# Kernel tuning notes

Measured on AMD Instinct MI355X. Metric: run time of the kernel, lower is better.

The kernel has to match this reference:

```python
import jax, jax.numpy as jnp
import numpy as np

B, INDIM, ENC, BOT, DEC = 2048, 20000, 512, 128, 512
EPS = 1e-5


def _bn(x, g, b):
    # BatchNorm1d in training mode: biased batch stats
    m = jnp.mean(x, axis=0)
    v = jnp.mean(jnp.square(x - m), axis=0)
    return (x - m) * jax.lax.rsqrt(v + EPS) * g + b


def setup_inputs() -> dict:
    key = jax.random.key(0)
    ks = jax.random.split(key, 8)
    s = 0.02  # small init scale keeps exp() outputs finite
    return {
        "x": jax.random.uniform(ks[0], (B, INDIM), dtype=jnp.float32),
        "bn0_g": jnp.ones((INDIM,), jnp.float32),
        "bn0_b": jnp.zeros((INDIM,), jnp.float32),
        "enc_W": jax.random.normal(ks[1], (ENC, INDIM), jnp.float32) * s,
        "enc_b": jnp.zeros((ENC,), jnp.float32),
        "bn1_g": jnp.ones((ENC,), jnp.float32),
        "bn1_b": jnp.zeros((ENC,), jnp.float32),
        "bot_W": jax.random.normal(ks[2], (BOT, ENC), jnp.float32) * s,
        "bot_b": jnp.zeros((BOT,), jnp.float32),
        "bn2_g": jnp.ones((BOT,), jnp.float32),
        "bn2_b": jnp.zeros((BOT,), jnp.float32),
        "dec_W": jax.random.normal(ks[3], (DEC, BOT), jnp.float32) * s,
        "dec_b": jnp.zeros((DEC,), jnp.float32),
        "o1_W": jax.random.normal(ks[4], (INDIM, DEC), jnp.float32) * s,
        "o1_b": jnp.zeros((INDIM,), jnp.float32),
        "o2_W": jax.random.normal(ks[5], (INDIM, DEC), jnp.float32) * s,
        "o2_b": jnp.zeros((INDIM,), jnp.float32),
        "o3_W": jax.random.normal(ks[6], (INDIM, DEC), jnp.float32) * s,
        "o3_b": jnp.zeros((INDIM,), jnp.float32),
    }


def reference(x, bn0_g, bn0_b, enc_W, enc_b, bn1_g, bn1_b, bot_W, bot_b,
              bn2_g, bn2_b, dec_W, dec_b, o1_W, o1_b, o2_W, o2_b, o3_W, o3_b):
    # row-sum / median normalization; diag-inverse @ x == x / s[:, None]
    row_sum = jnp.sum(x, axis=1)                     # [B]
    s = row_sum / jnp.median(row_sum)                # [B]
    h = jnp.log1p(x / s[:, None])                    # log(inv(diag(s)) @ x + 1)
    h = _bn(h, bn0_g, bn0_b)
    h = jax.nn.relu(h @ enc_W.T + enc_b)
    h = _bn(h, bn1_g, bn1_b)
    h = jax.nn.relu(h @ bot_W.T + bot_b)
    h = _bn(h, bn2_g, bn2_b)
    h = jax.nn.relu(h @ dec_W.T + dec_b)
    M = jnp.exp(h @ o1_W.T + o1_b)
    M_loss = s[:, None] * M                          # diag(s) @ M
    pai = jax.nn.sigmoid(h @ o2_W.T + o2_b)
    theta = jnp.exp(h @ o3_W.T + o3_b)
    return pai, M, theta, M_loss
```

## Files before the change

### kernel.cpp

```cpp
#include <hip/hip_runtime.h>
#include <hip/hip_bf16.h>
#include <math.h>

#define B_    2048
#define IND   20000
#define ENCN  512
#define BOTN  128
#define DECN  512
#define KP1   20480
#define NP    20224
#define SPLITK 16
#define KSTEP1 20
#define SPLITK2 4
#define BNEPS 1e-5f

typedef __hip_bfloat16 bf16;
typedef __bf16 bf16x8 __attribute__((ext_vector_type(8)));
typedef float f32x4 __attribute__((ext_vector_type(4)));
typedef unsigned short u16;

__device__ __forceinline__ u16 f2bfu(float f) {
  __hip_bfloat16 h = __float2bfloat16(f);
  return *reinterpret_cast<u16*>(&h);
}

__device__ __forceinline__ void st_b64_bf16(void* p, f32x4 v) {
  union { u16 u[4]; uint2 d; } o;
  o.u[0] = f2bfu(v[0]); o.u[1] = f2bfu(v[1]);
  o.u[2] = f2bfu(v[2]); o.u[3] = f2bfu(v[3]);
  *(uint2*)p = o.d;
}

__device__ __forceinline__ void gload_lds16(const bf16* g, bf16* l) {
  __builtin_amdgcn_global_load_lds(
      (const __attribute__((address_space(1))) void*)g,
      (__attribute__((address_space(3))) void*)l, 16, 0, 0);
}

__global__ void rowsum_k(const float* __restrict__ x, float* __restrict__ row_sum) {
  const int row = blockIdx.x;
  const f32x4* xr = (const f32x4*)(x + (size_t)row * IND);
  float s = 0.f;
  for (int i = threadIdx.x; i < IND / 4; i += 256) {
    f32x4 v = xr[i];
    s += (v[0] + v[1]) + (v[2] + v[3]);
  }
#pragma unroll
  for (int o = 32; o > 0; o >>= 1) s += __shfl_down(s, o, 64);
  __shared__ float ws4[4];
  if ((threadIdx.x & 63) == 0) ws4[threadIdx.x >> 6] = s;
  __syncthreads();
  if (threadIdx.x == 0) row_sum[row] = (ws4[0] + ws4[1]) + (ws4[2] + ws4[3]);
}

__global__ void median_scale_k(const float* __restrict__ row_sum,
                               float* __restrict__ sArr, float* __restrict__ invs) {
  __shared__ float v[B_];
  const int tid = threadIdx.x;
  v[tid] = row_sum[tid];
  v[tid + 1024] = row_sum[tid + 1024];
  __syncthreads();
  for (int k = 2; k <= B_; k <<= 1) {
    for (int j = k >> 1; j > 0; j >>= 1) {
      for (int i = tid; i < B_; i += 1024) {
        int ixj = i ^ j;
        if (ixj > i) {
          bool up = ((i & k) == 0);
          float a = v[i], b = v[ixj];
          if ((a > b) == up) { v[i] = b; v[ixj] = a; }
        }
      }
      __syncthreads();
    }
  }
  float med = 0.5f * (v[B_ / 2 - 1] + v[B_ / 2]);
  for (int i = tid; i < B_; i += 1024) {
    float rs = row_sum[i];
    sArr[i] = rs / med;
    invs[i] = med / rs;
  }
}

__global__ void pass2_k(const float* __restrict__ x, const float* __restrict__ invs,
                        bf16* __restrict__ L, float* __restrict__ part_s,
                        float* __restrict__ part_q) {
  const int c0 = (blockIdx.x * 256 + threadIdx.x) * 4;
  const int rblk = blockIdx.y;
  const int r0 = rblk * 32;
  const bool valid = (c0 < IND);
  f32x4 sum = {0.f, 0.f, 0.f, 0.f}, sq = {0.f, 0.f, 0.f, 0.f};
  for (int r = r0; r < r0 + 32; ++r) {
    f32x4 lv = {0.f, 0.f, 0.f, 0.f};
    if (valid) {
      f32x4 v = *(const f32x4*)(x + (size_t)r * IND + c0);
      float iv = invs[r];
      lv[0] = log1pf(v[0] * iv); lv[1] = log1pf(v[1] * iv);
      lv[2] = log1pf(v[2] * iv); lv[3] = log1pf(v[3] * iv);
      sum += lv; sq += lv * lv;
    }
    ushort4 o;
    o.x = f2bfu(lv[0]); o.y = f2bfu(lv[1]); o.z = f2bfu(lv[2]); o.w = f2bfu(lv[3]);
    *(ushort4*)((u16*)L + (size_t)r * KP1 + c0) = o;
  }
  if (valid) {
    *(f32x4*)(part_s + (size_t)rblk * KP1 + c0) = sum;
    *(f32x4*)(part_q + (size_t)rblk * KP1 + c0) = sq;
  }
}

__global__ void finalize_bn_k(const float* __restrict__ part_s, const float* __restrict__ part_q,
                              const float* __restrict__ g, const float* __restrict__ b,
                              float* __restrict__ scale, float* __restrict__ shift) {
  int c = blockIdx.x * 256 + threadIdx.x;
  if (c >= IND) return;
  float s = 0.f, q = 0.f;
  for (int z = 0; z < 64; ++z) {
    s += part_s[(size_t)z * KP1 + c];
    q += part_q[(size_t)z * KP1 + c];
  }
  const float invN = 1.f / (float)B_;
  float mean = s * invN;
  float var = q * invN - mean * mean;
  float sc = g[c] * rsqrtf(var + BNEPS);
  scale[c] = sc;
  shift[c] = b[c] - mean * sc;
}

__global__ void prepw_k(const float* __restrict__ encW, const float* __restrict__ enc_b,
                        const float* __restrict__ scale0, const float* __restrict__ shift0,
                        bf16* __restrict__ Wp, float* __restrict__ bias1) {
  const int e = blockIdx.x;
  float local = 0.f;
  for (int j0 = threadIdx.x * 4; j0 < KP1; j0 += 1024) {
    ushort4 o;
    if (j0 < IND) {
      f32x4 w = *(const f32x4*)(encW + (size_t)e * IND + j0);
      f32x4 sc = *(const f32x4*)(scale0 + j0);
      f32x4 sh = *(const f32x4*)(shift0 + j0);
      local += sh[0] * w[0] + sh[1] * w[1] + sh[2] * w[2] + sh[3] * w[3];
      o.x = f2bfu(w[0] * sc[0]); o.y = f2bfu(w[1] * sc[1]);
      o.z = f2bfu(w[2] * sc[2]); o.w = f2bfu(w[3] * sc[3]);
    } else {
      o.x = 0; o.y = 0; o.z = 0; o.w = 0;
    }
    *(ushort4*)((u16*)Wp + (size_t)e * KP1 + j0) = o;
  }
#pragma unroll
  for (int o = 32; o > 0; o >>= 1) local += __shfl_down(local, o, 64);
  __shared__ float red[4];
  if ((threadIdx.x & 63) == 0) red[threadIdx.x >> 6] = local;
  __syncthreads();
  if (threadIdx.x == 0) bias1[e] = enc_b[e] + ((red[0] + red[1]) + (red[2] + red[3]));
}

__global__ __launch_bounds__(512, 2)
void gemm1_k(const bf16* __restrict__ A, const bf16* __restrict__ Bm,
             float* __restrict__ Cp) {
  extern __shared__ __align__(16) bf16 smem[];
  bf16* Asm = smem;
  bf16* Bsm = smem + 32768;
  const int tid = threadIdx.x;
  const int lane = tid & 63;
  const int wave = tid >> 6;
  const int wr = wave >> 2;
  const int wc = wave & 3;

  const int bid = blockIdx.x;
  const int swz = (bid & 7) * 32 + (bid >> 3);
  const int xm = swz & 7;
  const int rest = swz >> 3;
  const int yn = rest & 1;
  const int z = rest >> 1;
  const int m0 = xm * 256;
  const int n0 = yn * 256;
  const int kbeg = z * KSTEP1 * 64;

  const int srow = tid >> 3;
  const int schunk = (tid & 7) ^ (srow & 7);
  const bf16* gA = A + (size_t)(m0 + srow) * KP1 + kbeg + schunk * 8;
  const bf16* gB = Bm + (size_t)(n0 + srow) * KP1 + kbeg + schunk * 8;
  const int dst1 = tid * 8;

  const int lrow = lane & 15;
  const int kq = lane >> 4;
  const int rsw = lrow & 7;

  f32x4 acc[8][4] = {};
  bf16x8 bfv[4][2];

  auto SA = [&](int kt, int half) {
    const bf16* g = gA + (size_t)(half * 128) * KP1 + (size_t)kt * 64;
    bf16* l = Asm + (((kt & 1) * 2 + half) << 13) + dst1;
    gload_lds16(g, l);
    gload_lds16(g + (size_t)64 * KP1, l + 4096);
  };
  auto SB = [&](int kt, int half) {
    const bf16* g = gB + (size_t)(half * 128) * KP1 + (size_t)kt * 64;
    bf16* l = Bsm + (((kt & 1) * 2 + half) << 13) + dst1;
    gload_lds16(g, l);
    gload_lds16(g + (size_t)64 * KP1, l + 4096);
  };
  auto DSA = [&](int slot, int p, bf16x8 af[2][2]) {
#pragma unroll
    for (int i = 0; i < 2; ++i) {
      const int m = 2 * p + i;
      const int base = ((slot * 2 + (m >> 2)) * 128 + (m & 3) * 32 + wr * 16 + lrow) * 64;
#pragma unroll
      for (int kk = 0; kk < 2; ++kk)
        af[i][kk] = *(const bf16x8*)(&Asm[base + (((kk * 4 + kq) ^ rsw) << 3)]);
    }
  };
  auto DSB = [&](int slot) {
#pragma unroll
    for (int n = 0; n < 4; ++n) {
      const int base = ((slot * 2 + (wc >> 1)) * 128 + (wc & 1) * 64 + n * 16 + lrow) * 64;
#pragma unroll
      for (int kk = 0; kk < 2; ++kk)
        bfv[n][kk] = *(const bf16x8*)(&Bsm[base + (((kk * 4 + kq) ^ rsw) << 3)]);
    }
  };
  auto MF = [&](int p, bf16x8 af[2][2]) {
    __builtin_amdgcn_s_setprio(1);
#pragma unroll
    for (int i = 0; i < 2; ++i)
#pragma unroll
      for (int n = 0; n < 4; ++n)
#pragma unroll
        for (int kk = 0; kk < 2; ++kk)
          acc[2 * p + i][n] = __builtin_amdgcn_mfma_f32_16x16x32_bf16(
              bfv[n][kk], af[i][kk], acc[2 * p + i][n], 0, 0, 0);
    __builtin_amdgcn_s_setprio(0);
  };

  SA(0, 0); SA(0, 1); SB(0, 0); SB(0, 1);
  SB(1, 0); SB(1, 1); SA(1, 0);
  asm volatile("s_waitcnt vmcnt(6)" ::: "memory");
  __builtin_amdgcn_s_barrier();

  const int iters = KSTEP1 >> 1;
  for (int t = 0; t < iters; ++t) {
    const int e = 2 * t;
    const bool last = (t == iters - 1);
    bf16x8 af[2][2];
    DSB(0); DSA(0, 0, af);
    SA(e + 1, 1);
    __builtin_amdgcn_s_barrier();
    MF(0, af);
    __builtin_amdgcn_s_barrier();
    DSA(0, 1, af);
    if (!last) SB(e + 2, 0);
    __builtin_amdgcn_s_barrier();
    MF(1, af);
    __builtin_amdgcn_s_barrier();
    DSA(0, 2, af);
    if (!last) SB(e + 2, 1);
    __builtin_amdgcn_s_barrier();
    MF(2, af);
    __builtin_amdgcn_s_barrier();
    DSA(0, 3, af);
    if (!last) SA(e + 2, 0);
    if (last) { asm volatile("s_waitcnt vmcnt(0)" ::: "memory"); }
    else      { asm volatile("s_waitcnt vmcnt(6)" ::: "memory"); }
    __builtin_amdgcn_s_barrier();
    MF(3, af);
    __builtin_amdgcn_s_barrier();
    DSB(1); DSA(1, 0, af);
    if (!last) SA(e + 2, 1);
    __builtin_amdgcn_s_barrier();
    MF(0, af);
    __builtin_amdgcn_s_barrier();
    DSA(1, 1, af);
    if (!last) SB(e + 3, 0);
    __builtin_amdgcn_s_barrier();
    MF(1, af);
    __builtin_amdgcn_s_barrier();
    DSA(1, 2, af);
    if (!last) SB(e + 3, 1);
    __builtin_amdgcn_s_barrier();
    MF(2, af);
    __builtin_amdgcn_s_barrier();
    DSA(1, 3, af);
    if (!last) SA(e + 3, 0);
    if (last) { asm volatile("s_waitcnt vmcnt(0)" ::: "memory"); }
    else      { asm volatile("s_waitcnt vmcnt(6)" ::: "memory"); }
    __builtin_amdgcn_s_barrier();
    MF(3, af);
    __builtin_amdgcn_s_barrier();
  }

  float* o0 = Cp + (size_t)z * ((size_t)B_ * ENCN);
  const int gcolb = n0 + wc * 64 + kq * 4;
#pragma unroll
  for (int m = 0; m < 8; ++m) {
    const int grow = m0 + m * 32 + wr * 16 + lrow;
#pragma unroll
    for (int n = 0; n < 4; ++n) {
      const int gcol = gcolb + n * 16;
      *(f32x4*)(&o0[(size_t)grow * ENCN + gcol]) = acc[m][n];
    }
  }
}

__global__ __launch_bounds__(512, 2)
void gemm_out_k(const bf16* __restrict__ A, const bf16* __restrict__ Wall,
                const float* __restrict__ b0, const float* __restrict__ b1,
                const float* __restrict__ b2,
                const float* __restrict__ sArr, float* __restrict__ out) {
  extern __shared__ __align__(16) bf16 smem[];
  bf16* Asm = smem;
  bf16* Bsm = smem + 32768;
  const int tid = threadIdx.x;
  const int lane = tid & 63;
  const int wave = tid >> 6;
  const int wr = wave >> 2;
  const int wc = wave & 3;

  const int bid = blockIdx.x;
  const int swz = (bid & 7) * 237 + (bid >> 3);
  const int g = swz / 632;
  const int r2 = swz - g * 632;
  const int xm = r2 & 7;
  const int yn = r2 >> 3;
  const int m0 = xm * 256;
  const int n0 = yn * 256;

  const bf16* Bm = Wall + (size_t)g * ((size_t)NP * ENCN);
  const float* bg = (g == 0) ? b0 : (g == 1) ? b1 : b2;
  const size_t OFF = (size_t)B_ * IND;
  float* o0 = out + (size_t)g * OFF;
  float* o1 = out + 3 * OFF;

  const int srow = tid >> 3;
  const int schunk = (tid & 7) ^ (srow & 7);
  const bf16* gA = A + (size_t)(m0 + srow) * ENCN + schunk * 8;
  const bf16* gB = Bm + (size_t)(n0 + srow) * ENCN + schunk * 8;
  const int dst1 = tid * 8;

  const int lrow = lane & 15;
  const int kq = lane >> 4;
  const int rsw = lrow & 7;

  f32x4 acc[8][4] = {};
  bf16x8 bfv[4][2];

  auto SA = [&](int kt, int half) {
    const bf16* g_ = gA + (size_t)(half * 128) * ENCN + (size_t)kt * 64;
    bf16* l = Asm + (((kt & 1) * 2 + half) << 13) + dst1;
    gload_lds16(g_, l);
    gload_lds16(g_ + (size_t)64 * ENCN, l + 4096);
  };
  auto SB = [&](int kt, int half) {
    const bf16* g_ = gB + (size_t)(half * 128) * ENCN + (size_t)kt * 64;
    bf16* l = Bsm + (((kt & 1) * 2 + half) << 13) + dst1;
    gload_lds16(g_, l);
    gload_lds16(g_ + (size_t)64 * ENCN, l + 4096);
  };
  auto DSA = [&](int slot, int p, bf16x8 af[2][2]) {
#pragma unroll
    for (int i = 0; i < 2; ++i) {
      const int m = 2 * p + i;
      const int base = ((slot * 2 + (m >> 2)) * 128 + (m & 3) * 32 + wr * 16 + lrow) * 64;
#pragma unroll
      for (int kk = 0; kk < 2; ++kk)
        af[i][kk] = *(const bf16x8*)(&Asm[base + (((kk * 4 + kq) ^ rsw) << 3)]);
    }
  };
  auto DSB = [&](int slot) {
#pragma unroll
    for (int n = 0; n < 4; ++n) {
      const int base = ((slot * 2 + (wc >> 1)) * 128 + (wc & 1) * 64 + n * 16 + lrow) * 64;
#pragma unroll
      for (int kk = 0; kk < 2; ++kk)
        bfv[n][kk] = *(const bf16x8*)(&Bsm[base + (((kk * 4 + kq) ^ rsw) << 3)]);
    }
  };
  auto MF = [&](int p, bf16x8 af[2][2]) {
    __builtin_amdgcn_s_setprio(1);
#pragma unroll
    for (int i = 0; i < 2; ++i)
#pragma unroll
      for (int n = 0; n < 4; ++n)
#pragma unroll
        for (int kk = 0; kk < 2; ++kk)
          acc[2 * p + i][n] = __builtin_amdgcn_mfma_f32_16x16x32_bf16(
              bfv[n][kk], af[i][kk], acc[2 * p + i][n], 0, 0, 0);
    __builtin_amdgcn_s_setprio(0);
  };

  SA(0, 0); SA(0, 1); SB(0, 0); SB(0, 1);
  SB(1, 0); SB(1, 1); SA(1, 0);
  asm volatile("s_waitcnt vmcnt(6)" ::: "memory");
  __builtin_amdgcn_s_barrier();

  const int iters = 4;
  for (int t = 0; t < iters; ++t) {
    const int e = 2 * t;
    const bool last = (t == iters - 1);
    bf16x8 af[2][2];
    DSB(0); DSA(0, 0, af);
    SA(e + 1, 1);
    __builtin_amdgcn_s_barrier();
    MF(0, af);
    __builtin_amdgcn_s_barrier();
    DSA(0, 1, af);
    if (!last) SB(e + 2, 0);
    __builtin_amdgcn_s_barrier();
    MF(1, af);
    __builtin_amdgcn_s_barrier();
    DSA(0, 2, af);
    if (!last) SB(e + 2, 1);
    __builtin_amdgcn_s_barrier();
    MF(2, af);
    __builtin_amdgcn_s_barrier();
    DSA(0, 3, af);
    if (!last) SA(e + 2, 0);
    if (last) { asm volatile("s_waitcnt vmcnt(0)" ::: "memory"); }
    else      { asm volatile("s_waitcnt vmcnt(6)" ::: "memory"); }
    __builtin_amdgcn_s_barrier();
    MF(3, af);
    __builtin_amdgcn_s_barrier();
    DSB(1); DSA(1, 0, af);
    if (!last) SA(e + 2, 1);
    __builtin_amdgcn_s_barrier();
    MF(0, af);
    __builtin_amdgcn_s_barrier();
    DSA(1, 1, af);
    if (!last) SB(e + 3, 0);
    __builtin_amdgcn_s_barrier();
    MF(1, af);
    __builtin_amdgcn_s_barrier();
    DSA(1, 2, af);
    if (!last) SB(e + 3, 1);
    __builtin_amdgcn_s_barrier();
    MF(2, af);
    __builtin_amdgcn_s_barrier();
    DSA(1, 3, af);
    if (!last) SA(e + 3, 0);
    if (last) { asm volatile("s_waitcnt vmcnt(0)" ::: "memory"); }
    else      { asm volatile("s_waitcnt vmcnt(6)" ::: "memory"); }
    __builtin_amdgcn_s_barrier();
    MF(3, af);
    __builtin_amdgcn_s_barrier();
  }

  const int gcolb = n0 + wc * 64 + kq * 4;
#pragma unroll
  for (int m = 0; m < 8; ++m) {
    const int grow = m0 + m * 32 + wr * 16 + lrow;
    float srow_s = 0.f;
    if (g == 1) srow_s = sArr[grow];
#pragma unroll
    for (int n = 0; n < 4; ++n) {
      const int gcol = gcolb + n * 16;
      if (gcol < IND) {
        f32x4 bb = *(const f32x4*)(&bg[gcol]);
        f32x4 t = acc[m][n] + bb;
        f32x4 r;
        if (g == 0) {
#pragma unroll
          for (int j = 0; j < 4; ++j) r[j] = 1.f / (1.f + __expf(-t[j]));
          *(f32x4*)(&o0[(size_t)grow * IND + gcol]) = r;
        } else {
#pragma unroll
          for (int j = 0; j < 4; ++j) r[j] = __expf(t[j]);
          *(f32x4*)(&o0[(size_t)grow * IND + gcol]) = r;
          if (g == 1) {
            f32x4 rl;
#pragma unroll
            for (int j = 0; j < 4; ++j) rl[j] = srow_s * r[j];
            *(f32x4*)(&o1[(size_t)grow * IND + gcol]) = rl;
          }
        }
      }
    }
  }
}

template <int EPI>
__global__ __launch_bounds__(256, 2)
void gemm_mid_k(const float* __restrict__ A, int lda,
                const float* __restrict__ scl, const float* __restrict__ sft,
                const float* __restrict__ W, int ldb,
                const float* __restrict__ bias,
                float* __restrict__ outP, bf16* __restrict__ outB, int ldo) {
  __shared__ __align__(16) bf16 As[128 * 64];
  __shared__ __align__(16) bf16 Bs[128 * 64];
  const int tid = threadIdx.x;
  const int lane = tid & 63;
  const int wave = tid >> 6;
  const int wr = wave >> 1, wc = wave & 1;
  const int m0 = blockIdx.x * 128;
  const int n0 = blockIdx.y * 128;
  const int z = blockIdx.z;
  const int kbeg = z * 128;
  const int lrow = lane & 15;
  const int kq = lane >> 4;
  const int scol = lrow * 4;
  const int srow0 = wave * 32 + kq;

  f32x4 acc[4][4] = {};
  for (int ks = 0; ks < 2; ++ks) {
    const int kb = kbeg + ks * 64;
    f32x4 sc4 = *(const f32x4*)(scl + kb + scol);
    f32x4 sf4 = *(const f32x4*)(sft + kb + scol);
#pragma unroll
    for (int i = 0; i < 8; ++i) {
      const int r = srow0 + i * 4;
      const int byte = r * 128 + (((lrow >> 1) ^ (r & 7)) << 4) + ((lrow & 1) << 3);
      f32x4 a = *(const f32x4*)(A + (size_t)(m0 + r) * lda + kb + scol);
      a = a * sc4 + sf4;
      st_b64_bf16((char*)As + byte, a);
      f32x4 b = *(const f32x4*)(W + (size_t)(n0 + r) * ldb + kb + scol);
      st_b64_bf16((char*)Bs + byte, b);
    }
    __syncthreads();
#pragma unroll
    for (int kk = 0; kk < 2; ++kk) {
      const int kc = kk * 4 + kq;
      bf16x8 af[4], bfv[4];
#pragma unroll
      for (int m = 0; m < 4; ++m) {
        const int row = wr * 64 + m * 16 + lrow;
        af[m] = *(const bf16x8*)(&As[row * 64 + (((kc ^ (row & 7)) & 7) << 3)]);
      }
#pragma unroll
      for (int n = 0; n < 4; ++n) {
        const int row = wc * 64 + n * 16 + lrow;
        bfv[n] = *(const bf16x8*)(&Bs[row * 64 + (((kc ^ (row & 7)) & 7) << 3)]);
      }
#pragma unroll
      for (int m = 0; m < 4; ++m)
#pragma unroll
        for (int n = 0; n < 4; ++n)
          acc[m][n] = __builtin_amdgcn_mfma_f32_16x16x32_bf16(bfv[n], af[m], acc[m][n], 0, 0, 0);
    }
    __syncthreads();
  }

  const int growb = m0 + wr * 64 + lrow;
  const int gcolb = n0 + wc * 64 + kq * 4;
#pragma unroll
  for (int m = 0; m < 4; ++m) {
    const int grow = growb + m * 16;
#pragma unroll
    for (int n = 0; n < 4; ++n) {
      const int gcol = gcolb + n * 16;
      if (EPI == 0) {
        float* op = outP + (size_t)z * ((size_t)B_ * ldo);
        *(f32x4*)(&op[(size_t)grow * ldo + gcol]) = acc[m][n];
      } else {
        f32x4 t = acc[m][n] + *(const f32x4*)(&bias[gcol]);
        f32x4 r;
#pragma unroll
        for (int j = 0; j < 4; ++j) r[j] = fmaxf(t[j], 0.f);
        st_b64_bf16((u16*)outB + (size_t)grow * ldo + gcol, r);
      }
    }
  }
}

__global__ void reduce1c_k(const float* __restrict__ Cp, const float* __restrict__ bias1,
                           float* __restrict__ C1, float* __restrict__ ps,
                           float* __restrict__ pq) {
  const int b = blockIdx.x;
  const int t = threadIdx.x;
  const int c4 = (t & 127) * 4;
  const int rs = t >> 7;
  f32x4 bb = *(const f32x4*)(bias1 + c4);
  f32x4 sum = {0.f, 0.f, 0.f, 0.f}, sq = {0.f, 0.f, 0.f, 0.f};
#pragma unroll
  for (int rr = 0; rr < 4; ++rr) {
    const int row = b * 8 + rs + rr * 2;
    f32x4 v = {0.f, 0.f, 0.f, 0.f};
#pragma unroll
    for (int z = 0; z < SPLITK; ++z)
      v += *(const f32x4*)(Cp + (size_t)z * (B_ * ENCN) + (size_t)row * ENCN + c4);
    v += bb;
    f32x4 r;
#pragma unroll
    for (int j = 0; j < 4; ++j) r[j] = fmaxf(v[j], 0.f);
    *(f32x4*)(C1 + (size_t)row * ENCN + c4) = r;
    sum += r; sq += r * r;
  }
  __shared__ f32x4 ls[2][128], lq[2][128];
  ls[rs][t & 127] = sum; lq[rs][t & 127] = sq;
  __syncthreads();
  if (t < 128) {
    f32x4 s = ls[0][t] + ls[1][t];
    f32x4 q = lq[0][t] + lq[1][t];
    *(f32x4*)(ps + (size_t)b * ENCN + t * 4) = s;
    *(f32x4*)(pq + (size_t)b * ENCN + t * 4) = q;
  }
}

__global__ void reduce2c_k(const float* __restrict__ Cp2, const float* __restrict__ bias,
                           float* __restrict__ C2, float* __restrict__ ps,
                           float* __restrict__ pq) {
  const int b = blockIdx.x;
  const int t = threadIdx.x;
  const int c4 = (t & 31) * 4;
  const int rs = t >> 5;
  f32x4 bb = *(const f32x4*)(bias + c4);
  f32x4 sum = {0.f, 0.f, 0.f, 0.f}, sq = {0.f, 0.f, 0.f, 0.f};
#pragma unroll
  for (int rr = 0; rr < 2; ++rr) {
    const int row = b * 16 + rs + rr * 8;
    f32x4 v = {0.f, 0.f, 0.f, 0.f};
#pragma unroll
    for (int z = 0; z < SPLITK2; ++z)
      v += *(const f32x4*)(Cp2 + (size_t)z * (B_ * BOTN) + (size_t)row * BOTN + c4);
    v += bb;
    f32x4 r;
#pragma unroll
    for (int j = 0; j < 4; ++j) r[j] = fmaxf(v[j], 0.f);
    *(f32x4*)(C2 + (size_t)row * BOTN + c4) = r;
    sum += r; sq += r * r;
  }
  __shared__ f32x4 ls[8][32], lq[8][32];
  ls[rs][t & 31] = sum; lq[rs][t & 31] = sq;
  __syncthreads();
  if (t < 32) {
    f32x4 s = {0.f, 0.f, 0.f, 0.f}, q = {0.f, 0.f, 0.f, 0.f};
#pragma unroll
    for (int k = 0; k < 8; ++k) { s += ls[k][t]; q += lq[k][t]; }
    *(f32x4*)(ps + (size_t)b * BOTN + t * 4) = s;
    *(f32x4*)(pq + (size_t)b * BOTN + t * 4) = q;
  }
}

__global__ void colfin_k(const float* __restrict__ ps, const float* __restrict__ pq,
                         const float* __restrict__ g, const float* __restrict__ b,
                         float* __restrict__ scale, float* __restrict__ shift,
                         int C, int nPart) {
  const int cl = threadIdx.x & 63;
  const int pg = threadIdx.x >> 6;
  const int c = blockIdx.x * 64 + cl;
  float s = 0.f, q = 0.f;
  for (int p = pg; p < nPart; p += 4) {
    s += ps[(size_t)p * C + c];
    q += pq[(size_t)p * C + c];
  }
  __shared__ float ls[4][64], lq[4][64];
  ls[pg][cl] = s; lq[pg][cl] = q;
  __syncthreads();
  if (pg == 0) {
    s = (ls[0][cl] + ls[1][cl]) + (ls[2][cl] + ls[3][cl]);
    q = (lq[0][cl] + lq[1][cl]) + (lq[2][cl] + lq[3][cl]);
    const float invN = 1.f / (float)B_;
    float mean = s * invN;
    float var = q * invN - mean * mean;
    float sc = g[c] * rsqrtf(var + BNEPS);
    scale[c] = sc;
    shift[c] = b[c] - mean * sc;
  }
}

__global__ void cvt_all_k(const float* __restrict__ W0, const float* __restrict__ W1,
                          const float* __restrict__ W2, bf16* __restrict__ Wb) {
  const size_t SEG = (size_t)NP * 512;
  const size_t idx = ((size_t)blockIdx.x * 256 + threadIdx.x) * 4;
  const int seg = (int)(idx / SEG);
  const size_t rem = idx - (size_t)seg * SEG;
  const int e = (int)(rem >> 9);
  const float* src = (seg == 0) ? W0 : (seg == 1) ? W1 : W2;
  ushort4 o;
  if (e < IND) {
    f32x4 v = *(const f32x4*)(src + rem);
    o.x = f2bfu(v[0]); o.y = f2bfu(v[1]); o.z = f2bfu(v[2]); o.w = f2bfu(v[3]);
  } else {
    o.x = 0; o.y = 0; o.z = 0; o.w = 0;
  }
  *(ushort4*)((u16*)Wb + idx) = o;
}

extern "C" void kernel_launch(void* const* d_in, const int* in_sizes, int n_in,
                              void* d_out, int out_size, void* d_ws, size_t ws_size,
                              hipStream_t stream) {
  const float* x     = (const float*)d_in[0];
  const float* bn0_g = (const float*)d_in[1];
  const float* bn0_b = (const float*)d_in[2];
  const float* enc_W = (const float*)d_in[3];
  const float* enc_b = (const float*)d_in[4];
  const float* bn1_g = (const float*)d_in[5];
  const float* bn1_b = (const float*)d_in[6];
  const float* bot_W = (const float*)d_in[7];
  const float* bot_b = (const float*)d_in[8];
  const float* bn2_g = (const float*)d_in[9];
  const float* bn2_b = (const float*)d_in[10];
  const float* dec_W = (const float*)d_in[11];
  const float* dec_b = (const float*)d_in[12];
  const float* o1_W  = (const float*)d_in[13];
  const float* o1_b  = (const float*)d_in[14];
  const float* o2_W  = (const float*)d_in[15];
  const float* o2_b  = (const float*)d_in[16];
  const float* o3_W  = (const float*)d_in[17];
  const float* o3_b  = (const float*)d_in[18];

  char* wsb = (char*)d_ws;
  size_t off = 0;
  auto alloc = [&](size_t bytes) -> void* {
    void* p = wsb + off;
    off = (off + bytes + 255) & ~(size_t)255;
    return p;
  };
  float* row_sum = (float*)alloc(B_ * 4);
  float* sArr    = (float*)alloc(B_ * 4);
  float* invs    = (float*)alloc(B_ * 4);
  float* scale0  = (float*)alloc(IND * 4);
  float* shift0  = (float*)alloc(IND * 4);
  float* bias1   = (float*)alloc(ENCN * 4);
  float* scale1  = (float*)alloc(ENCN * 4);
  float* shift1  = (float*)alloc(ENCN * 4);
  float* scale2  = (float*)alloc(BOTN * 4);
  float* shift2  = (float*)alloc(BOTN * 4);
  float* ps1     = (float*)alloc(256 * ENCN * 4);
  float* pq1     = (float*)alloc(256 * ENCN * 4);
  float* ps2     = (float*)alloc(128 * BOTN * 4);
  float* pq2     = (float*)alloc(128 * BOTN * 4);
  float* C1      = (float*)alloc((size_t)B_ * ENCN * 4);
  float* C2f     = (float*)alloc((size_t)B_ * BOTN * 4);
  float* Cp2     = (float*)alloc((size_t)SPLITK2 * B_ * BOTN * 4);
  float* Cp      = (float*)alloc((size_t)SPLITK * B_ * ENCN * 4);
  bf16*  L       = (bf16*)alloc((size_t)B_ * KP1 * 2);
  bf16*  Wp      = (bf16*)alloc((size_t)ENCN * KP1 * 2);
  bf16*  h3      = (bf16*)alloc((size_t)B_ * DECN * 2);
  bf16*  Wall    = (bf16*)alloc((size_t)3 * NP * 512 * 2);
  float* part_s  = Cp;
  float* part_q  = Cp + (size_t)64 * KP1;

  hipFuncSetAttribute(reinterpret_cast<const void*>(gemm1_k),
                      hipFuncAttributeMaxDynamicSharedMemorySize, 131072);
  hipFuncSetAttribute(reinterpret_cast<const void*>(gemm_out_k),
                      hipFuncAttributeMaxDynamicSharedMemorySize, 131072);

  rowsum_k<<<B_, 256, 0, stream>>>(x, row_sum);
  median_scale_k<<<1, 1024, 0, stream>>>(row_sum, sArr, invs);

  pass2_k<<<dim3(KP1 / 1024, 64), 256, 0, stream>>>(x, invs, L, part_s, part_q);
  finalize_bn_k<<<(IND + 255) / 256, 256, 0, stream>>>(part_s, part_q, bn0_g, bn0_b,
                                                       scale0, shift0);

  prepw_k<<<ENCN, 256, 0, stream>>>(enc_W, enc_b, scale0, shift0, Wp, bias1);

  gemm1_k<<<256, 512, 131072, stream>>>(L, Wp, Cp);
  reduce1c_k<<<256, 256, 0, stream>>>(Cp, bias1, C1, ps1, pq1);
  colfin_k<<<ENCN / 64, 256, 0, stream>>>(ps1, pq1, bn1_g, bn1_b, scale1, shift1,
                                          ENCN, 256);

  gemm_mid_k<0><<<dim3(16, 1, SPLITK2), 256, 0, stream>>>(
      C1, ENCN, scale1, shift1, bot_W, ENCN, nullptr, Cp2, nullptr, BOTN);
  reduce2c_k<<<128, 256, 0, stream>>>(Cp2, bot_b, C2f, ps2, pq2);
  colfin_k<<<BOTN / 64, 256, 0, stream>>>(ps2, pq2, bn2_g, bn2_b, scale2, shift2,
                                          BOTN, 128);
  gemm_mid_k<1><<<dim3(16, 4, 1), 256, 0, stream>>>(
      C2f, BOTN, scale2, shift2, dec_W, BOTN, dec_b, nullptr, h3, DECN);

  cvt_all_k<<<(3 * NP * 512) / 1024, 256, 0, stream>>>(o2_W, o1_W, o3_W, Wall);

  float* out = (float*)d_out;
  gemm_out_k<<<1896, 512, 131072, stream>>>(h3, Wall, o2_b, o1_b, o3_b, sArr, out);
}
```

Measured before the change: 681.0 us.

## Fuse output weight conversion into pass2, split output GEMM per head, rank-based median

Folds the bf16 conversion of the three output weight matrices into the log1p/BN-stats kernel as extra blocks, so both memory-bound passes share one launch. The first GEMM and the output GEMM now use one templated kernel, and the single combined output GEMM becomes three launches, one per head. The bitonic sort in the median kernel is replaced by an O(N) rank count per element with a single barrier. Separate per-head launches add tail and launch overhead, and the combined pass2 kernel has more uneven per-block work.

```diff
diff --git a/kernel.cpp b/kernel.cpp
--- a/kernel.cpp
+++ b/kernel.cpp
@@ -13,6 +13,7 @@
 #define KSTEP1 20
 #define SPLITK2 4
 #define BNEPS 1e-5f
+#define WSEG  (NP * 512)
 
 typedef __hip_bfloat16 bf16;
 typedef __bf16 bf16x8 __attribute__((ext_vector_type(8)));
@@ -56,55 +57,81 @@
 __global__ void median_scale_k(const float* __restrict__ row_sum,
                                float* __restrict__ sArr, float* __restrict__ invs) {
   __shared__ float v[B_];
+  __shared__ float mv[2];
   const int tid = threadIdx.x;
   v[tid] = row_sum[tid];
   v[tid + 1024] = row_sum[tid + 1024];
   __syncthreads();
-  for (int k = 2; k <= B_; k <<= 1) {
-    for (int j = k >> 1; j > 0; j >>= 1) {
-      for (int i = tid; i < B_; i += 1024) {
-        int ixj = i ^ j;
-        if (ixj > i) {
-          bool up = ((i & k) == 0);
-          float a = v[i], b = v[ixj];
-          if ((a > b) == up) { v[i] = b; v[ixj] = a; }
-        }
-      }
-      __syncthreads();
-    }
-  }
-  float med = 0.5f * (v[B_ / 2 - 1] + v[B_ / 2]);
+  const float a = v[tid];
+  const float b = v[tid + 1024];
+  int ra = 0, rb = 0;
+  for (int j = 0; j < B_; ++j) {
+    float x = v[j];
+    ra += (x < a) | ((x == a) & (j < tid));
+    rb += (x < b) | ((x == b) & (j < tid + 1024));
+  }
+  if (ra == 1023) mv[0] = a;
+  if (ra == 1024) mv[1] = a;
+  if (rb == 1023) mv[0] = b;
+  if (rb == 1024) mv[1] = b;
+  __syncthreads();
+  const float med = 0.5f * (mv[0] + mv[1]);
   for (int i = tid; i < B_; i += 1024) {
-    float rs = row_sum[i];
+    float rs = v[i];
     sArr[i] = rs / med;
     invs[i] = med / rs;
   }
 }
 
-__global__ void pass2_k(const float* __restrict__ x, const float* __restrict__ invs,
-                        bf16* __restrict__ L, float* __restrict__ part_s,
-                        float* __restrict__ part_q) {
-  const int c0 = (blockIdx.x * 256 + threadIdx.x) * 4;
-  const int rblk = blockIdx.y;
-  const int r0 = rblk * 32;
-  const bool valid = (c0 < IND);
-  f32x4 sum = {0.f, 0.f, 0.f, 0.f}, sq = {0.f, 0.f, 0.f, 0.f};
-  for (int r = r0; r < r0 + 32; ++r) {
-    f32x4 lv = {0.f, 0.f, 0.f, 0.f};
+__global__ void pass2cvt_k(const float* __restrict__ x, const float* __restrict__ invs,
+                           bf16* __restrict__ L, float* __restrict__ part_s,
+                           float* __restrict__ part_q,
+                           const float* __restrict__ W0, const float* __restrict__ W1,
+                           const float* __restrict__ W2, bf16* __restrict__ Wall) {
+  const int b = blockIdx.x;
+  if (b < 1280) {
+    const int bx = b % 20;
+    const int rblk = b / 20;
+    const int c0 = (bx * 256 + threadIdx.x) * 4;
+    const int r0 = rblk * 32;
+    const bool valid = (c0 < IND);
+    f32x4 sum = {0.f, 0.f, 0.f, 0.f}, sq = {0.f, 0.f, 0.f, 0.f};
+    for (int r = r0; r < r0 + 32; ++r) {
+      f32x4 lv = {0.f, 0.f, 0.f, 0.f};
+      if (valid) {
+        f32x4 v = *(const f32x4*)(x + (size_t)r * IND + c0);
+        float iv = invs[r];
+        lv[0] = log1pf(v[0] * iv); lv[1] = log1pf(v[1] * iv);
+        lv[2] = log1pf(v[2] * iv); lv[3] = log1pf(v[3] * iv);
+        sum += lv; sq += lv * lv;
+      }
+      ushort4 o;
+      o.x = f2bfu(lv[0]); o.y = f2bfu(lv[1]); o.z = f2bfu(lv[2]); o.w = f2bfu(lv[3]);
+      *(ushort4*)((u16*)L + (size_t)r * KP1 + c0) = o;
+    }
     if (valid) {
-      f32x4 v = *(const f32x4*)(x + (size_t)r * IND + c0);
-      float iv = invs[r];
-      lv[0] = log1pf(v[0] * iv); lv[1] = log1pf(v[1] * iv);
-      lv[2] = log1pf(v[2] * iv); lv[3] = log1pf(v[3] * iv);
-      sum += lv; sq += lv * lv;
-    }
-    ushort4 o;
-    o.x = f2bfu(lv[0]); o.y = f2bfu(lv[1]); o.z = f2bfu(lv[2]); o.w = f2bfu(lv[3]);
-    *(ushort4*)((u16*)L + (size_t)r * KP1 + c0) = o;
-  }
-  if (valid) {
-    *(f32x4*)(part_s + (size_t)rblk * KP1 + c0) = sum;
-    *(f32x4*)(part_q + (size_t)rblk * KP1 + c0) = sq;
+      *(f32x4*)(part_s + (size_t)rblk * KP1 + c0) = sum;
+      *(f32x4*)(part_q + (size_t)rblk * KP1 + c0) = sq;
+    }
+  } else {
+    const long long TC = (long long)3 * WSEG / 4;
+    long long idx = (long long)(b - 1280) * 256 + threadIdx.x;
+    const long long stride = 1024 * 256;
+    for (; idx < TC; idx += stride) {
+      const long long e4 = idx * 4;
+      const int seg = (int)(e4 / WSEG);
+      const long long rem = e4 - (long long)seg * WSEG;
+      const int erow = (int)(rem >> 9);
+      const float* src = (seg == 0) ? W0 : (seg == 1) ? W1 : W2;
+      ushort4 o;
+      if (erow < IND) {
+        f32x4 v = *(const f32x4*)(src + rem);
+        o.x = f2bfu(v[0]); o.y = f2bfu(v[1]); o.z = f2bfu(v[2]); o.w = f2bfu(v[3]);
+      } else {
+        o.x = 0; o.y = 0; o.z = 0; o.w = 0;
+      }
+      *(ushort4*)((u16*)Wall + e4) = o;
+    }
   }
 }
 
@@ -153,9 +180,13 @@
   if (threadIdx.x == 0) bias1[e] = enc_b[e] + ((red[0] + red[1]) + (red[2] + red[3]));
 }
 
+template <int MODE>
 __global__ __launch_bounds__(512, 2)
-void gemm1_k(const bf16* __restrict__ A, const bf16* __restrict__ Bm,
-             float* __restrict__ Cp) {
+void gemm256(const bf16* __restrict__ A, const bf16* __restrict__ Bm,
+             int Kpad, int ksteps,
+             float* __restrict__ out0, float* __restrict__ out1,
+             const float* __restrict__ bias, const float* __restrict__ sArr,
+             int ldo, int Nlimit) {
   extern __shared__ __align__(16) bf16 smem[];
   bf16* Asm = smem;
   bf16* Bsm = smem + 32768;
@@ -165,20 +196,22 @@
   const int wr = wave >> 2;
   const int wc = wave & 3;
 
+  const int nwg = gridDim.x;
+  const int q8 = nwg >> 3;
   const int bid = blockIdx.x;
-  const int swz = (bid & 7) * 32 + (bid >> 3);
+  const int swz = (bid & 7) * q8 + (bid >> 3);
   const int xm = swz & 7;
   const int rest = swz >> 3;
-  const int yn = rest & 1;
-  const int z = rest >> 1;
+  int yn, z;
+  if (MODE == 0) { yn = rest & 1; z = rest >> 1; } else { yn = rest; z = 0; }
   const int m0 = xm * 256;
   const int n0 = yn * 256;
-  const int kbeg = z * KSTEP1 * 64;
+  const int kbeg = z * ksteps * 64;
 
   const int srow = tid >> 3;
   const int schunk = (tid & 7) ^ (srow & 7);
-  const bf16* gA = A + (size_t)(m0 + srow) * KP1 + kbeg + schunk * 8;
-  const bf16* gB = Bm + (size_t)(n0 + srow) * KP1 + kbeg + schunk * 8;
+  const bf16* gA = A + (size_t)(m0 + srow) * Kpad + kbeg + schunk * 8;
+  const bf16* gB = Bm + (size_t)(n0 + srow) * Kpad + kbeg + schunk * 8;
   const int dst1 = tid * 8;
 
   const int lrow = lane & 15;
@@ -189,16 +222,16 @@
   bf16x8 bfv[4][2];
 
   auto SA = [&](int kt, int half) {
-    const bf16* g = gA + (size_t)(half * 128) * KP1 + (size_t)kt * 64;
+    const bf16* g = gA + (size_t)(half * 128) * Kpad + (size_t)kt * 64;
     bf16* l = Asm + (((kt & 1) * 2 + half) << 13) + dst1;
     gload_lds16(g, l);
-    gload_lds16(g + (size_t)64 * KP1, l + 4096);
+    gload_lds16(g + (size_t)64 * Kpad, l + 4096);
   };
   auto SB = [&](int kt, int half) {
-    const bf16* g = gB + (size_t)(half * 128) * KP1 + (size_t)kt * 64;
+    const bf16* g = gB + (size_t)(half * 128) * Kpad + (size_t)kt * 64;
     bf16* l = Bsm + (((kt & 1) * 2 + half) << 13) + dst1;
     gload_lds16(g, l);
-    gload_lds16(g + (size_t)64 * KP1, l + 4096);
+    gload_lds16(g + (size_t)64 * Kpad, l + 4096);
   };
   auto DSA = [&](int slot, int p, bf16x8 af[2][2]) {
 #pragma unroll
@@ -237,7 +270,7 @@
   asm volatile("s_waitcnt vmcnt(6)" ::: "memory");
   __builtin_amdgcn_s_barrier();
 
-  const int iters = KSTEP1 >> 1;
+  const int iters = ksteps >> 1;
   for (int t = 0; t < iters; ++t) {
     const int e = 2 * t;
     const bool last = (t == iters - 1);
@@ -288,188 +321,40 @@
     __builtin_amdgcn_s_barrier();
   }
 
-  float* o0 = Cp + (size_t)z * ((size_t)B_ * ENCN);
-  const int gcolb = n0 + wc * 64 + kq * 4;
-#pragma unroll
-  for (int m = 0; m < 8; ++m) {
-    const int grow = m0 + m * 32 + wr * 16 + lrow;
-#pragma unroll
-    for (int n = 0; n < 4; ++n) {
-      const int gcol = gcolb + n * 16;
-      *(f32x4*)(&o0[(size_t)grow * ENCN + gcol]) = acc[m][n];
-    }
-  }
-}
-
-__global__ __launch_bounds__(512, 2)
-void gemm_out_k(const bf16* __restrict__ A, const bf16* __restrict__ Wall,
-                const float* __restrict__ b0, const float* __restrict__ b1,
-                const float* __restrict__ b2,
-                const float* __restrict__ sArr, float* __restrict__ out) {
-  extern __shared__ __align__(16) bf16 smem[];
-  bf16* Asm = smem;
-  bf16* Bsm = smem + 32768;
-  const int tid = threadIdx.x;
-  const int lane = tid & 63;
-  const int wave = tid >> 6;
-  const int wr = wave >> 2;
-  const int wc = wave & 3;
-
-  const int bid = blockIdx.x;
-  const int swz = (bid & 7) * 237 + (bid >> 3);
-  const int g = swz / 632;
-  const int r2 = swz - g * 632;
-  const int xm = r2 & 7;
-  const int yn = r2 >> 3;
-  const int m0 = xm * 256;
-  const int n0 = yn * 256;
-
-  const bf16* Bm = Wall + (size_t)g * ((size_t)NP * ENCN);
-  const float* bg = (g == 0) ? b0 : (g == 1) ? b1 : b2;
-  const size_t OFF = (size_t)B_ * IND;
-  float* o0 = out + (size_t)g * OFF;
-  float* o1 = out + 3 * OFF;
-
-  const int srow = tid >> 3;
-  const int schunk = (tid & 7) ^ (srow & 7);
-  const bf16* gA = A + (size_t)(m0 + srow) * ENCN + schunk * 8;
-  const bf16* gB = Bm + (size_t)(n0 + srow) * ENCN + schunk * 8;
-  const int dst1 = tid * 8;
-
-  const int lrow = lane & 15;
-  const int kq = lane >> 4;
-  const int rsw = lrow & 7;
-
-  f32x4 acc[8][4] = {};
-  bf16x8 bfv[4][2];
-
-  auto SA = [&](int kt, int half) {
-    const bf16* g_ = gA + (size_t)(half * 128) * ENCN + (size_t)kt * 64;
-    bf16* l = Asm + (((kt & 1) * 2 + half) << 13) + dst1;
-    gload_lds16(g_, l);
-    gload_lds16(g_ + (size_t)64 * ENCN, l + 4096);
-  };
-  auto SB = [&](int kt, int half) {
-    const bf16* g_ = gB + (size_t)(half * 128) * ENCN + (size_t)kt * 64;
-    bf16* l = Bsm + (((kt & 1) * 2 + half) << 13) + dst1;
-    gload_lds16(g_, l);
-    gload_lds16(g_ + (size_t)64 * ENCN, l + 4096);
-  };
-  auto DSA = [&](int slot, int p, bf16x8 af[2][2]) {
-#pragma unroll
-    for (int i = 0; i < 2; ++i) {
-      const int m = 2 * p + i;
-      const int base = ((slot * 2 + (m >> 2)) * 128 + (m & 3) * 32 + wr * 16 + lrow) * 64;
-#pragma unroll
-      for (int kk = 0; kk < 2; ++kk)
-        af[i][kk] = *(const bf16x8*)(&Asm[base + (((kk * 4 + kq) ^ rsw) << 3)]);
-    }
-  };
-  auto DSB = [&](int slot) {
-#pragma unroll
-    for (int n = 0; n < 4; ++n) {
-      const int base = ((slot * 2 + (wc >> 1)) * 128 + (wc & 1) * 64 + n * 16 + lrow) * 64;
-#pragma unroll
-      for (int kk = 0; kk < 2; ++kk)
-        bfv[n][kk] = *(const bf16x8*)(&Bsm[base + (((kk * 4 + kq) ^ rsw) << 3)]);
-    }
-  };
-  auto MF = [&](int p, bf16x8 af[2][2]) {
-    __builtin_amdgcn_s_setprio(1);
-#pragma unroll
-    for (int i = 0; i < 2; ++i)
-#pragma unroll
-      for (int n = 0; n < 4; ++n)
-#pragma unroll
-        for (int kk = 0; kk < 2; ++kk)
-          acc[2 * p + i][n] = __builtin_amdgcn_mfma_f32_16x16x32_bf16(
-              bfv[n][kk], af[i][kk], acc[2 * p + i][n], 0, 0, 0);
-    __builtin_amdgcn_s_setprio(0);
-  };
-
-  SA(0, 0); SA(0, 1); SB(0, 0); SB(0, 1);
-  SB(1, 0); SB(1, 1); SA(1, 0);
-  asm volatile("s_waitcnt vmcnt(6)" ::: "memory");
-  __builtin_amdgcn_s_barrier();
-
-  const int iters = 4;
-  for (int t = 0; t < iters; ++t) {
-    const int e = 2 * t;
-    const bool last = (t == iters - 1);
-    bf16x8 af[2][2];
-    DSB(0); DSA(0, 0, af);
-    SA(e + 1, 1);
-    __builtin_amdgcn_s_barrier();
-    MF(0, af);
-    __builtin_amdgcn_s_barrier();
-    DSA(0, 1, af);
-    if (!last) SB(e + 2, 0);
-    __builtin_amdgcn_s_barrier();
-    MF(1, af);
-    __builtin_amdgcn_s_barrier();
-    DSA(0, 2, af);
-    if (!last) SB(e + 2, 1);
-    __builtin_amdgcn_s_barrier();
-    MF(2, af);
-    __builtin_amdgcn_s_barrier();
-    DSA(0, 3, af);
-    if (!last) SA(e + 2, 0);
-    if (last) { asm volatile("s_waitcnt vmcnt(0)" ::: "memory"); }
-    else      { asm volatile("s_waitcnt vmcnt(6)" ::: "memory"); }
-    __builtin_amdgcn_s_barrier();
-    MF(3, af);
-    __builtin_amdgcn_s_barrier();
-    DSB(1); DSA(1, 0, af);
-    if (!last) SA(e + 2, 1);
-    __builtin_amdgcn_s_barrier();
-    MF(0, af);
-    __builtin_amdgcn_s_barrier();
-    DSA(1, 1, af);
-    if (!last) SB(e + 3, 0);
-    __builtin_amdgcn_s_barrier();
-    MF(1, af);
-    __builtin_amdgcn_s_barrier();
-    DSA(1, 2, af);
-    if (!last) SB(e + 3, 1);
-    __builtin_amdgcn_s_barrier();
-    MF(2, af);
-    __builtin_amdgcn_s_barrier();
-    DSA(1, 3, af);
-    if (!last) SA(e + 3, 0);
-    if (last) { asm volatile("s_waitcnt vmcnt(0)" ::: "memory"); }
-    else      { asm volatile("s_waitcnt vmcnt(6)" ::: "memory"); }
-    __builtin_amdgcn_s_barrier();
-    MF(3, af);
-    __builtin_amdgcn_s_barrier();
-  }
-
+  float* o0 = out0;
+  if (MODE == 0) o0 += (size_t)z * ((size_t)B_ * ldo);
   const int gcolb = n0 + wc * 64 + kq * 4;
 #pragma unroll
   for (int m = 0; m < 8; ++m) {
     const int grow = m0 + m * 32 + wr * 16 + lrow;
     float srow_s = 0.f;
-    if (g == 1) srow_s = sArr[grow];
+    if (MODE == 2) srow_s = sArr[grow];
 #pragma unroll
     for (int n = 0; n < 4; ++n) {
       const int gcol = gcolb + n * 16;
-      if (gcol < IND) {
-        f32x4 bb = *(const f32x4*)(&bg[gcol]);
-        f32x4 t = acc[m][n] + bb;
+      f32x4 v = acc[m][n];
+      if (MODE == 0) {
+        *(f32x4*)(&o0[(size_t)grow * ldo + gcol]) = v;
+      } else if (gcol < Nlimit) {
+        f32x4 bb = *(const f32x4*)(&bias[gcol]);
+        f32x4 t = v + bb;
         f32x4 r;
-        if (g == 0) {
+        if (MODE == 1) {
 #pragma unroll
           for (int j = 0; j < 4; ++j) r[j] = 1.f / (1.f + __expf(-t[j]));
-          *(f32x4*)(&o0[(size_t)grow * IND + gcol]) = r;
+          *(f32x4*)(&o0[(size_t)grow * ldo + gcol]) = r;
+        } else if (MODE == 2) {
+#pragma unroll
+          for (int j = 0; j < 4; ++j) r[j] = __expf(t[j]);
+          *(f32x4*)(&o0[(size_t)grow * ldo + gcol]) = r;
+          f32x4 rl;
+#pragma unroll
+          for (int j = 0; j < 4; ++j) rl[j] = srow_s * r[j];
+          *(f32x4*)(&out1[(size_t)grow * ldo + gcol]) = rl;
         } else {
 #pragma unroll
           for (int j = 0; j < 4; ++j) r[j] = __expf(t[j]);
-          *(f32x4*)(&o0[(size_t)grow * IND + gcol]) = r;
-          if (g == 1) {
-            f32x4 rl;
-#pragma unroll
-            for (int j = 0; j < 4; ++j) rl[j] = srow_s * r[j];
-            *(f32x4*)(&o1[(size_t)grow * IND + gcol]) = rl;
-          }
+          *(f32x4*)(&o0[(size_t)grow * ldo + gcol]) = r;
         }
       }
     }
@@ -653,24 +538,6 @@
     scale[c] = sc;
     shift[c] = b[c] - mean * sc;
   }
-}
-
-__global__ void cvt_all_k(const float* __restrict__ W0, const float* __restrict__ W1,
-                          const float* __restrict__ W2, bf16* __restrict__ Wb) {
-  const size_t SEG = (size_t)NP * 512;
-  const size_t idx = ((size_t)blockIdx.x * 256 + threadIdx.x) * 4;
-  const int seg = (int)(idx / SEG);
-  const size_t rem = idx - (size_t)seg * SEG;
-  const int e = (int)(rem >> 9);
-  const float* src = (seg == 0) ? W0 : (seg == 1) ? W1 : W2;
-  ushort4 o;
-  if (e < IND) {
-    f32x4 v = *(const f32x4*)(src + rem);
-    o.x = f2bfu(v[0]); o.y = f2bfu(v[1]); o.z = f2bfu(v[2]); o.w = f2bfu(v[3]);
-  } else {
-    o.x = 0; o.y = 0; o.z = 0; o.w = 0;
-  }
-  *(ushort4*)((u16*)Wb + idx) = o;
 }
 
 extern "C" void kernel_launch(void* const* d_in, const int* in_sizes, int n_in,
@@ -724,25 +591,34 @@
   bf16*  L       = (bf16*)alloc((size_t)B_ * KP1 * 2);
   bf16*  Wp      = (bf16*)alloc((size_t)ENCN * KP1 * 2);
   bf16*  h3      = (bf16*)alloc((size_t)B_ * DECN * 2);
-  bf16*  Wall    = (bf16*)alloc((size_t)3 * NP * 512 * 2);
+  bf16*  Wall    = (bf16*)alloc((size_t)3 * WSEG * 2);
   float* part_s  = Cp;
   float* part_q  = Cp + (size_t)64 * KP1;
-
-  hipFuncSetAttribute(reinterpret_cast<const void*>(gemm1_k),
+  bf16* w_o2 = Wall;
+  bf16* w_o1 = Wall + (size_t)WSEG;
+  bf16* w_o3 = Wall + (size_t)2 * WSEG;
+
+  hipFuncSetAttribute(reinterpret_cast<const void*>(gemm256<0>),
                       hipFuncAttributeMaxDynamicSharedMemorySize, 131072);
-  hipFuncSetAttribute(reinterpret_cast<const void*>(gemm_out_k),
+  hipFuncSetAttribute(reinterpret_cast<const void*>(gemm256<1>),
+                      hipFuncAttributeMaxDynamicSharedMemorySize, 131072);
+  hipFuncSetAttribute(reinterpret_cast<const void*>(gemm256<2>),
+                      hipFuncAttributeMaxDynamicSharedMemorySize, 131072);
+  hipFuncSetAttribute(reinterpret_cast<const void*>(gemm256<3>),
                       hipFuncAttributeMaxDynamicSharedMemorySize, 131072);
 
   rowsum_k<<<B_, 256, 0, stream>>>(x, row_sum);
   median_scale_k<<<1, 1024, 0, stream>>>(row_sum, sArr, invs);
 
-  pass2_k<<<dim3(KP1 / 1024, 64), 256, 0, stream>>>(x, invs, L, part_s, part_q);
+  pass2cvt_k<<<2304, 256, 0, stream>>>(x, invs, L, part_s, part_q,
+                                       o2_W, o1_W, o3_W, Wall);
   finalize_bn_k<<<(IND + 255) / 256, 256, 0, stream>>>(part_s, part_q, bn0_g, bn0_b,
                                                        scale0, shift0);
 
   prepw_k<<<ENCN, 256, 0, stream>>>(enc_W, enc_b, scale0, shift0, Wp, bias1);
 
-  gemm1_k<<<256, 512, 131072, stream>>>(L, Wp, Cp);
+  gemm256<0><<<8 * 2 * SPLITK, 512, 131072, stream>>>(
+      L, Wp, KP1, KSTEP1, Cp, nullptr, nullptr, nullptr, ENCN, ENCN);
   reduce1c_k<<<256, 256, 0, stream>>>(Cp, bias1, C1, ps1, pq1);
   colfin_k<<<ENCN / 64, 256, 0, stream>>>(ps1, pq1, bn1_g, bn1_b, scale1, shift1,
                                           ENCN, 256);
@@ -755,8 +631,13 @@
   gemm_mid_k<1><<<dim3(16, 4, 1), 256, 0, stream>>>(
       C2f, BOTN, scale2, shift2, dec_W, BOTN, dec_b, nullptr, h3, DECN);
 
-  cvt_all_k<<<(3 * NP * 512) / 1024, 256, 0, stream>>>(o2_W, o1_W, o3_W, Wall);
-
   float* out = (float*)d_out;
-  gemm_out_k<<<1896, 512, 131072, stream>>>(h3, Wall, o2_b, o1_b, o3_b, sArr, out);
-}
+  const size_t OFF = (size_t)B_ * IND;
+  const int onwg = 8 * (NP / 256);
+  gemm256<1><<<onwg, 512, 131072, stream>>>(
+      h3, w_o2, 512, 8, out, nullptr, o2_b, nullptr, IND, IND);
+  gemm256<2><<<onwg, 512, 131072, stream>>>(
+      h3, w_o1, 512, 8, out + OFF, out + 3 * OFF, o1_b, sArr, IND, IND);
+  gemm256<3><<<onwg, 512, 131072, stream>>>(
+      h3, w_o3, 512, 8, out + 2 * OFF, nullptr, o3_b, nullptr, IND, IND);
+}
```

Result: slower. 783.6 us (+15.1%).
